# Performance work log

Measured on AMD Instinct MI355X. Metric: run time of the kernel, lower is better.

## Reference

```python
import jax, jax.numpy as jnp
import numpy as np
import math

FACTOR = 5  # module default

def setup_inputs() -> dict:
    key = jax.random.key(0)
    kq, kk, kv, ki = jax.random.split(key, 4)
    B, L, S, H, D = 2, 4096, 4096, 8, 64
    u_part = min(FACTOR * math.ceil(math.log(L)), S)  # 45: sampled keys per query
    return {
        "queries": jax.random.normal(kq, (B, L, H, D), jnp.float32),
        "keys": jax.random.normal(kk, (B, S, H, D), jnp.float32),
        "values": jax.random.normal(kv, (B, S, H, D), jnp.float32),
        "index_sample": jax.random.randint(ki, (L, u_part), 0, S),
    }

def reference(queries, keys, values, index_sample):
    # queries: [B,L,H,D], keys/values: [B,S,H,D], index_sample: [L,u_part]
    B, L, H, D = queries.shape
    S = keys.shape[1]
    Q = jnp.transpose(queries, (0, 2, 1, 3))  # [B,H,L,D]
    K = jnp.transpose(keys, (0, 2, 1, 3))     # [B,H,S,D]
    V = jnp.transpose(values, (0, 2, 1, 3))   # [B,H,S,D]
    U_part = min(FACTOR * math.ceil(math.log(S)), L)  # n_top queries (static)

    # --- _prob_QK: sample keys, sparsity measure M, top-k queries ---
    K_sample = K[:, :, index_sample, :]  # gather -> [B,H,L,u_part,D]
    QK_sample = jnp.einsum('bhld,bhlud->bhlu', Q, K_sample)  # [B,H,L,u_part]
    M = QK_sample.max(axis=-1) - QK_sample.sum(axis=-1) / S  # [B,H,L]
    _, M_top = jax.lax.top_k(M, U_part)                      # [B,H,U_part]
    Q_reduce = jnp.take_along_axis(Q, M_top[..., None], axis=2)  # [B,H,U_part,D]
    scores = jnp.einsum('bhud,bhsd->bhus', Q_reduce, K)          # [B,H,U_part,S]

    # --- mask_flag=False branch: plain scaled softmax attention ---
    scale = 1.0 / math.sqrt(D)
    attn = jax.nn.softmax(scores * scale, axis=-1)  # [B,H,U_part,S]
    context = jnp.einsum('bhus,bhsd->bhud', attn, V)  # [B,H,U_part,D]
    return context, attn
```

## Files before the change

kernel.cpp:

```cpp
#include <hip/hip_runtime.h>

#define BB 2
#define LL 4096
#define SS 4096
#define HH 8
#define DD 64
#define UU 45
#define SCALE 0.125f

__global__ __launch_bounds__(256) void k_compute_M(
    const float* __restrict__ q, const float* __restrict__ k,
    const int* __restrict__ idx, float* __restrict__ M) {
  __shared__ int sidx[16 * UU];
  int tid = threadIdx.x;
  int bh = blockIdx.x & 15;
  int l0 = (blockIdx.x >> 4) << 4;
  for (int i = tid; i < 16 * UU; i += 256) sidx[i] = idx[(long)l0 * UU + i];
  __syncthreads();

  int slot = tid >> 4;
  int sub  = tid & 15;
  int l = l0 + slot;
  int b = bh >> 3, h = bh & 7;

  const float4* qp = (const float4*)(q + (((long)b * LL + l) * HH + h) * DD);
  float4 qq = qp[sub];
  const float* kb = k + (long)b * SS * HH * DD + h * DD;

  float mx = -INFINITY, sm = 0.f;
  #pragma unroll 5
  for (int u = 0; u < UU; ++u) {
    int s = sidx[slot * UU + u];
    float4 kk4 = ((const float4*)(kb + (long)s * (HH * DD)))[sub];
    float p = qq.x * kk4.x + qq.y * kk4.y + qq.z * kk4.z + qq.w * kk4.w;
    #pragma unroll
    for (int off = 8; off; off >>= 1) p += __shfl_xor(p, off, 16);
    mx = fmaxf(mx, p);
    sm += p;
  }
  if (sub == 0) M[(long)bh * LL + l] = mx - sm * (1.0f / SS);
}

__global__ __launch_bounds__(256) void k_topk(
    const float* __restrict__ M, int* __restrict__ Mtop) {
  __shared__ unsigned keys[LL];
  __shared__ int hist[256];
  __shared__ int wsum[4];
  __shared__ int sh_bin, sh_gtwin;
  __shared__ int ccount, ecount;
  __shared__ unsigned cand_key[64];
  __shared__ int cand_idx[64];
  __shared__ int elist[LL];

  int bh = blockIdx.x, tid = threadIdx.x;
  int lane = tid & 63, w = tid >> 6;
  const float* m = M + (long)bh * LL;
  for (int i = tid; i < LL; i += 256) {
    union { float f; unsigned u; } cv; cv.f = m[i];
    keys[i] = (cv.u & 0x80000000u) ? ~cv.u : (cv.u | 0x80000000u);
  }
  if (tid == 0) { ccount = 0; ecount = 0; }
  __syncthreads();

  unsigned prefix = 0, pmask = 0;
  int need = UU, above = 0;

  for (int shift = 24; shift >= 0; shift -= 8) {
    hist[tid] = 0;
    __syncthreads();
    #pragma unroll
    for (int j = 0; j < 16; ++j) {
      unsigned kk = keys[tid + (j << 8)];
      if ((kk & pmask) == prefix) atomicAdd(&hist[(kk >> shift) & 255], 1);
    }
    __syncthreads();
    int v = hist[tid];
    int sfx = v;
    #pragma unroll
    for (int st = 1; st < 64; st <<= 1) {
      int o = __shfl_down(sfx, st, 64);
      if (lane + st < 64) sfx += o;
    }
    if (lane == 0) wsum[w] = sfx;
    __syncthreads();
    for (int t = w + 1; t < 4; ++t) sfx += wsum[t];
    int gt = sfx - v;
    if (gt < need && sfx >= need) {
      sh_bin = tid;
      sh_gtwin = gt;
    }
    __syncthreads();
    prefix |= ((unsigned)sh_bin << shift);
    pmask  |= (255u << shift);
    need  -= sh_gtwin;
    above += sh_gtwin;
    __syncthreads();
  }
  unsigned T = prefix;

  #pragma unroll
  for (int j = 0; j < 16; ++j) {
    int i = tid + (j << 8);
    unsigned kk = keys[i];
    if (kk > T)      { int p = atomicAdd(&ccount, 1); cand_key[p] = kk; cand_idx[p] = i; }
    else if (kk == T){ int p = atomicAdd(&ecount, 1); elist[p] = i; }
  }
  __syncthreads();
  int nc = ccount, ne = ecount;
  for (int t = tid; t < nc; t += 256) {
    unsigned kk = cand_key[t]; int ii = cand_idx[t]; int r = 0;
    for (int j = 0; j < nc; ++j)
      r += (cand_key[j] > kk) || (cand_key[j] == kk && cand_idx[j] < ii);
    Mtop[bh * UU + r] = ii;
  }
  for (int t = tid; t < ne; t += 256) {
    int ii = elist[t]; int r = 0;
    for (int j = 0; j < ne; ++j) r += (elist[j] < ii);
    if (r < need) Mtop[bh * UU + above + r] = ii;
  }
}

__global__ __launch_bounds__(256) void k_scores(
    const float* __restrict__ q, const float* __restrict__ k,
    const int* __restrict__ Mtop, float* __restrict__ attn) {
  __shared__ float qr[UU * DD];
  int bh = blockIdx.y;
  int b = bh >> 3, h = bh & 7;
  for (int i = threadIdx.x; i < UU * DD; i += 256) {
    int u = i >> 6, d = i & 63;
    int l = Mtop[bh * UU + u];
    qr[i] = q[(((long)b * LL + l) * HH + h) * DD + d];
  }
  __syncthreads();
  int s = blockIdx.x * 256 + threadIdx.x;
  float4 kr[16];
  const float4* kp = (const float4*)(k + (((long)b * SS + s) * HH + h) * DD);
  #pragma unroll
  for (int j = 0; j < 16; ++j) kr[j] = kp[j];
  for (int u = 0; u < UU; ++u) {
    const float4* qp = (const float4*)(qr + u * DD);
    float acc = 0.f;
    #pragma unroll
    for (int j = 0; j < 16; ++j) {
      float4 qq = qp[j];
      acc += qq.x * kr[j].x + qq.y * kr[j].y + qq.z * kr[j].z + qq.w * kr[j].w;
    }
    attn[((long)bh * UU + u) * SS + s] = acc * SCALE;
  }
}

__global__ __launch_bounds__(256) void k_softmax(float* __restrict__ attn) {
  __shared__ float red[256];
  long row = blockIdx.x;
  float* a = attn + row * SS;
  float v[16];
  float mx = -INFINITY;
  #pragma unroll
  for (int j = 0; j < 16; ++j) {
    v[j] = a[j * 256 + threadIdx.x];
    mx = fmaxf(mx, v[j]);
  }
  red[threadIdx.x] = mx;
  __syncthreads();
  for (int st = 128; st; st >>= 1) {
    if (threadIdx.x < st) red[threadIdx.x] = fmaxf(red[threadIdx.x], red[threadIdx.x + st]);
    __syncthreads();
  }
  mx = red[0];
  __syncthreads();
  float sm = 0.f;
  #pragma unroll
  for (int j = 0; j < 16; ++j) {
    v[j] = __expf(v[j] - mx);
    sm += v[j];
  }
  red[threadIdx.x] = sm;
  __syncthreads();
  for (int st = 128; st; st >>= 1) {
    if (threadIdx.x < st) red[threadIdx.x] += red[threadIdx.x + st];
    __syncthreads();
  }
  float inv = 1.0f / red[0];
  #pragma unroll
  for (int j = 0; j < 16; ++j) a[j * 256 + threadIdx.x] = v[j] * inv;
}

__global__ __launch_bounds__(256) void k_context_part(
    const float* __restrict__ attn, const float* __restrict__ v,
    float* __restrict__ part, int nch) {
  __shared__ float smem[4 * UU * DD];
  int ch = blockIdx.x, bh = blockIdx.y;
  int b = bh >> 3, h = bh & 7;
  int tid = threadIdx.x;
  int ln = tid & 63, w = tid >> 6;
  int chunk = SS / nch;
  int s0 = ch * chunk;
  int nsub = chunk >> 7;

  float acc[UU];
  #pragma unroll
  for (int u = 0; u < UU; ++u) acc[u] = 0.f;

  const float* vb = v + (long)b * SS * HH * DD + h * DD + ln;

  for (int sub = 0; sub < nsub; ++sub) {
    int sb = s0 + (sub << 7);
    __syncthreads();
    for (int i = tid; i < UU * 128; i += 256) {
      int u = i >> 7, si = i & 127;
      smem[si * 52 + u] = attn[((long)bh * UU + u) * SS + sb + si];
    }
    __syncthreads();
    #pragma unroll 2
    for (int j = 0; j < 32; ++j) {
      int sl = (j << 2) + w;
      float vd = vb[(long)(sb + sl) * (HH * DD)];
      const float* ar = smem + sl * 52;
      #pragma unroll
      for (int g = 0; g < 11; ++g) {
        float4 aa = *(const float4*)(ar + g * 4);
        acc[g * 4 + 0] += aa.x * vd;
        acc[g * 4 + 1] += aa.y * vd;
        acc[g * 4 + 2] += aa.z * vd;
        acc[g * 4 + 3] += aa.w * vd;
      }
      acc[44] += ar[44] * vd;
    }
  }

  __syncthreads();
  #pragma unroll
  for (int u = 0; u < UU; ++u) smem[(w * UU + u) * DD + ln] = acc[u];
  __syncthreads();
  long base = ((long)bh * nch + ch) * (UU * DD);
  for (int i = tid; i < UU * DD; i += 256)
    part[base + i] = smem[i] + smem[UU * DD + i] + smem[2 * UU * DD + i] + smem[3 * UU * DD + i];
}

__global__ __launch_bounds__(256) void k_context_reduce(
    const float* __restrict__ part, float* __restrict__ ctx, int nch) {
  int g = blockIdx.x * 256 + threadIdx.x;
  int bh = g / (UU * DD);
  int r  = g - bh * (UU * DD);
  float s = 0.f;
  for (int ch = 0; ch < nch; ++ch)
    s += part[((long)bh * nch + ch) * (UU * DD) + r];
  ctx[g] = s;
}

__global__ __launch_bounds__(256) void k_context_fb(
    const float* __restrict__ attn, const float* __restrict__ v,
    float* __restrict__ ctx) {
  __shared__ float red[4][DD];
  int row = blockIdx.x;
  int bh = row / UU;
  int b = bh >> 3, h = bh & 7;
  int lane = threadIdx.x & 63;
  int grp = threadIdx.x >> 6;
  const float* a = attn + (long)row * SS;
  float acc = 0.f;
  for (int s = grp; s < SS; s += 4)
    acc += a[s] * v[(((long)b * SS + s) * HH + h) * DD + lane];
  red[grp][lane] = acc;
  __syncthreads();
  if (grp == 0)
    ctx[(long)row * DD + lane] = red[0][lane] + red[1][lane] + red[2][lane] + red[3][lane];
}

extern "C" void kernel_launch(void* const* d_in, const int* in_sizes, int n_in,
                              void* d_out, int out_size, void* d_ws, size_t ws_size,
                              hipStream_t stream) {
  const float* q   = (const float*)d_in[0];
  const float* k   = (const float*)d_in[1];
  const float* v   = (const float*)d_in[2];
  const int*   idx = (const int*)d_in[3];

  float* out  = (float*)d_out;
  float* ctx  = out;
  float* attn = out + (long)BB * HH * UU * DD;

  float* M    = attn;
  int*   Mtop = (int*)ctx;

  k_compute_M<<<BB * HH * LL / 16, 256, 0, stream>>>(q, k, idx, M);
  k_topk<<<BB * HH, 256, 0, stream>>>(M, Mtop);
  k_scores<<<dim3(SS / 256, BB * HH), 256, 0, stream>>>(q, k, Mtop, attn);
  k_softmax<<<BB * HH * UU, 256, 0, stream>>>(attn);

  size_t per_chunk = (size_t)BB * HH * UU * DD * sizeof(float);
  int nch = 0;
  for (int c = 32; c >= 1; c >>= 1)
    if (ws_size >= per_chunk * (size_t)c) { nch = c; break; }
  if (nch) {
    k_context_part<<<dim3(nch, BB * HH), 256, 0, stream>>>(attn, v, (float*)d_ws, nch);
    k_context_reduce<<<(BB * HH * UU * DD) / 256, 256, 0, stream>>>((const float*)d_ws, ctx, nch);
  } else {
    k_context_fb<<<BB * HH * UU, 256, 0, stream>>>(attn, v, ctx);
  }
}
```

Measured before the change: 122.7 us.

## Fuse softmax into score and context kernels via per-tile max/sum stats

Replaces the separate softmax pass with per-tile online-softmax statistics (max and exp-sum) computed in the score kernel. The context kernel merges the stats, normalizes attention on the fly while staging it into shared memory, and writes the normalized probabilities back. This removes one kernel launch and a full read-modify-write pass over the attention matrix. In exchange the score kernel gets extra shared memory for a score tile, and the workspace layout now reserves a fixed offset for the stats.

Measured after the change: 128.7 us. 1.05x slower.

```diff
diff --git a/kernel.cpp b/kernel.cpp
--- a/kernel.cpp
+++ b/kernel.cpp
@@ -7,6 +7,7 @@
 #define DD 64
 #define UU 45
 #define SCALE 0.125f
+#define NTILE 16
 
 __global__ __launch_bounds__(256) void k_compute_M(
     const float* __restrict__ q, const float* __restrict__ k,
@@ -120,6 +121,53 @@
   }
 }
 
+__global__ __launch_bounds__(256) void k_scores_stats(
+    const float* __restrict__ q, const float* __restrict__ k,
+    const int* __restrict__ Mtop, float* __restrict__ attn,
+    float2* __restrict__ stats) {
+  __shared__ float qr[UU * DD];
+  __shared__ float sc[UU][260];
+  int bh = blockIdx.y, tile = blockIdx.x;
+  int b = bh >> 3, h = bh & 7;
+  int tid = threadIdx.x;
+  for (int i = tid; i < UU * DD; i += 256) {
+    int u = i >> 6, d = i & 63;
+    int l = Mtop[bh * UU + u];
+    qr[i] = q[(((long)b * LL + l) * HH + h) * DD + d];
+  }
+  __syncthreads();
+  int s = tile * 256 + tid;
+  float4 kr[16];
+  const float4* kp = (const float4*)(k + (((long)b * SS + s) * HH + h) * DD);
+  #pragma unroll
+  for (int j = 0; j < 16; ++j) kr[j] = kp[j];
+  for (int u = 0; u < UU; ++u) {
+    const float4* qp = (const float4*)(qr + u * DD);
+    float acc = 0.f;
+    #pragma unroll
+    for (int j = 0; j < 16; ++j) {
+      float4 qq = qp[j];
+      acc += qq.x * kr[j].x + qq.y * kr[j].y + qq.z * kr[j].z + qq.w * kr[j].w;
+    }
+    acc *= SCALE;
+    sc[u][tid] = acc;
+    attn[((long)bh * UU + u) * SS + s] = acc;
+  }
+  __syncthreads();
+  int lane = tid & 63, w = tid >> 6;
+  for (int u = w; u < UU; u += 4) {
+    float a0 = sc[u][lane],       a1 = sc[u][lane + 64];
+    float a2 = sc[u][lane + 128], a3 = sc[u][lane + 192];
+    float mx = fmaxf(fmaxf(a0, a1), fmaxf(a2, a3));
+    #pragma unroll
+    for (int off = 32; off; off >>= 1) mx = fmaxf(mx, __shfl_xor(mx, off, 64));
+    float e = __expf(a0 - mx) + __expf(a1 - mx) + __expf(a2 - mx) + __expf(a3 - mx);
+    #pragma unroll
+    for (int off = 32; off; off >>= 1) e += __shfl_xor(e, off, 64);
+    if (lane == 0) stats[((long)bh * UU + u) * NTILE + tile] = make_float2(mx, e);
+  }
+}
+
 __global__ __launch_bounds__(256) void k_scores(
     const float* __restrict__ q, const float* __restrict__ k,
     const int* __restrict__ Mtop, float* __restrict__ attn) {
@@ -186,9 +234,10 @@
 }
 
 __global__ __launch_bounds__(256) void k_context_part(
-    const float* __restrict__ attn, const float* __restrict__ v,
-    float* __restrict__ part, int nch) {
+    float* __restrict__ attn, const float2* __restrict__ stats,
+    const float* __restrict__ v, float* __restrict__ part, int nch) {
   __shared__ float smem[4 * UU * DD];
+  __shared__ float gm[UU], gi[UU];
   int ch = blockIdx.x, bh = blockIdx.y;
   int b = bh >> 3, h = bh & 7;
   int tid = threadIdx.x;
@@ -197,6 +246,17 @@
   int s0 = ch * chunk;
   int nsub = chunk >> 7;
 
+  if (tid < UU) {
+    const float2* st = stats + ((long)bh * UU + tid) * NTILE;
+    float mx = -INFINITY;
+    #pragma unroll
+    for (int t = 0; t < NTILE; ++t) mx = fmaxf(mx, st[t].x);
+    float sm = 0.f;
+    #pragma unroll
+    for (int t = 0; t < NTILE; ++t) sm += st[t].y * __expf(st[t].x - mx);
+    gm[tid] = mx; gi[tid] = 1.0f / sm;
+  }
+
   float acc[UU];
   #pragma unroll
   for (int u = 0; u < UU; ++u) acc[u] = 0.f;
@@ -208,7 +268,10 @@
     __syncthreads();
     for (int i = tid; i < UU * 128; i += 256) {
       int u = i >> 7, si = i & 127;
-      smem[si * 52 + u] = attn[((long)bh * UU + u) * SS + sb + si];
+      long ga = ((long)bh * UU + u) * SS + sb + si;
+      float p = __expf(attn[ga] - gm[u]) * gi[u];
+      smem[si * 52 + u] = p;
+      attn[ga] = p;
     }
     __syncthreads();
     #pragma unroll 2
@@ -284,17 +347,24 @@
 
   k_compute_M<<<BB * HH * LL / 16, 256, 0, stream>>>(q, k, idx, M);
   k_topk<<<BB * HH, 256, 0, stream>>>(M, Mtop);
-  k_scores<<<dim3(SS / 256, BB * HH), 256, 0, stream>>>(q, k, Mtop, attn);
-  k_softmax<<<BB * HH * UU, 256, 0, stream>>>(attn);
-
-  size_t per_chunk = (size_t)BB * HH * UU * DD * sizeof(float);
+
+  size_t stats_bytes = (size_t)BB * HH * UU * NTILE * sizeof(float2);
+  size_t stats_off   = 131072;
+  size_t per_chunk   = (size_t)BB * HH * UU * DD * sizeof(float);
   int nch = 0;
   for (int c = 32; c >= 1; c >>= 1)
-    if (ws_size >= per_chunk * (size_t)c) { nch = c; break; }
+    if (ws_size >= stats_off + per_chunk * (size_t)c) { nch = c; break; }
+
   if (nch) {
-    k_context_part<<<dim3(nch, BB * HH), 256, 0, stream>>>(attn, v, (float*)d_ws, nch);
-    k_context_reduce<<<(BB * HH * UU * DD) / 256, 256, 0, stream>>>((const float*)d_ws, ctx, nch);
+    float2* stats = (float2*)d_ws;
+    float*  part  = (float*)((char*)d_ws + stats_off);
+    k_scores_stats<<<dim3(NTILE, BB * HH), 256, 0, stream>>>(q, k, Mtop, attn, stats);
+    k_context_part<<<dim3(nch, BB * HH), 256, 0, stream>>>(attn, stats, v, part, nch);
+    k_context_reduce<<<(BB * HH * UU * DD) / 256, 256, 0, stream>>>(part, ctx, nch);
   } else {
+    k_scores<<<dim3(SS / 256, BB * HH), 256, 0, stream>>>(q, k, Mtop, attn);
+    k_softmax<<<BB * HH * UU, 256, 0, stream>>>(attn);
     k_context_fb<<<BB * HH * UU, 256, 0, stream>>>(attn, v, ctx);
   }
-}
+  (void)stats_bytes;
+}
```

## Fuse scores, chunked softmax and context into one flash-style kernel with epilogue

Applied to the files above, without the earlier changes.

Replaces the separate scores, softmax, context-partial and reduce kernels with one fused kernel. Each block computes a 128-key chunk of scores, a local max and sum, unnormalized probabilities and partial context. A combined epilogue kernel then rescales attn rows and merges the partial contexts using the per-chunk stats. This removes the round trips of the attn matrix through global memory and two kernel launches. In exchange the attn rows are rewritten in a second pass, and the fused kernel launches only 512 blocks with heavy register use.

Measured after the change: 108.6 us, median of 2. 11.5% less time.

```diff
diff --git a/kernel.cpp b/kernel.cpp
--- a/kernel.cpp
+++ b/kernel.cpp
@@ -7,6 +7,8 @@
 #define DD 64
 #define UU 45
 #define SCALE 0.125f
+#define NCH 32
+#define CHK 128
 
 __global__ __launch_bounds__(256) void k_compute_M(
     const float* __restrict__ q, const float* __restrict__ k,
@@ -120,6 +122,157 @@
   }
 }
 
+__global__ __launch_bounds__(256) void k_fused(
+    const float* __restrict__ q, const float* __restrict__ k,
+    const float* __restrict__ v, const int* __restrict__ Mtop,
+    float* __restrict__ attn, float* __restrict__ part,
+    float2* __restrict__ stats) {
+  __shared__ float smem[4 * UU * DD];
+  __shared__ float gm[UU], gl[UU];
+  float* qr = smem;
+  float* sp = smem + UU * DD;
+
+  int ch = blockIdx.x, bh = blockIdx.y;
+  int b = bh >> 3, h = bh & 7;
+  int tid = threadIdx.x;
+  int lane = tid & 63, w = tid >> 6;
+  int s0 = ch * CHK;
+
+  for (int i = tid; i < UU * DD; i += 256) {
+    int u = i >> 6, d = i & 63;
+    int l = Mtop[bh * UU + u];
+    qr[i] = q[(((long)b * LL + l) * HH + h) * DD + d];
+  }
+  __syncthreads();
+
+  {
+    int sl = tid & 127, uh = tid >> 7;
+    float4 kr[16];
+    const float4* kp = (const float4*)(k + (((long)b * SS + s0 + sl) * HH + h) * DD);
+    #pragma unroll
+    for (int j = 0; j < 16; ++j) kr[j] = kp[j];
+    int u0 = uh ? 23 : 0, u1 = uh ? UU : 23;
+    for (int u = u0; u < u1; ++u) {
+      const float4* qp = (const float4*)(qr + u * DD);
+      float acc = 0.f;
+      #pragma unroll
+      for (int j = 0; j < 16; ++j) {
+        float4 qq = qp[j];
+        acc += qq.x * kr[j].x + qq.y * kr[j].y + qq.z * kr[j].z + qq.w * kr[j].w;
+      }
+      sp[sl * 52 + u] = acc * SCALE;
+    }
+  }
+  __syncthreads();
+
+  for (int u = w; u < UU; u += 4) {
+    float a0 = sp[lane * 52 + u];
+    float a1 = sp[(lane + 64) * 52 + u];
+    float mx = fmaxf(a0, a1);
+    #pragma unroll
+    for (int off = 32; off; off >>= 1) mx = fmaxf(mx, __shfl_xor(mx, off, 64));
+    if (lane == 0) gm[u] = mx;
+  }
+  __syncthreads();
+  for (int i = tid; i < UU * CHK; i += 256) {
+    int u = i >> 7, sl = i & 127;
+    float p = __expf(sp[sl * 52 + u] - gm[u]);
+    sp[sl * 52 + u] = p;
+    attn[((long)bh * UU + u) * SS + s0 + sl] = p;
+  }
+  __syncthreads();
+  for (int u = w; u < UU; u += 4) {
+    float a0 = sp[lane * 52 + u];
+    float a1 = sp[(lane + 64) * 52 + u];
+    float e = a0 + a1;
+    #pragma unroll
+    for (int off = 32; off; off >>= 1) e += __shfl_xor(e, off, 64);
+    if (lane == 0) gl[u] = e;
+  }
+
+  float acc[UU];
+  #pragma unroll
+  for (int u = 0; u < UU; ++u) acc[u] = 0.f;
+  const float* vb = v + (long)b * SS * HH * DD + h * DD + lane;
+  #pragma unroll 2
+  for (int j = 0; j < 32; ++j) {
+    int sl = (j << 2) + w;
+    float vd = vb[(long)(s0 + sl) * (HH * DD)];
+    const float* ar = sp + sl * 52;
+    #pragma unroll
+    for (int g = 0; g < 11; ++g) {
+      float4 aa = *(const float4*)(ar + g * 4);
+      acc[g * 4 + 0] += aa.x * vd;
+      acc[g * 4 + 1] += aa.y * vd;
+      acc[g * 4 + 2] += aa.z * vd;
+      acc[g * 4 + 3] += aa.w * vd;
+    }
+    acc[44] += ar[44] * vd;
+  }
+
+  __syncthreads();
+  #pragma unroll
+  for (int u = 0; u < UU; ++u) smem[(w * UU + u) * DD + lane] = acc[u];
+  __syncthreads();
+  long base = ((long)bh * NCH + ch) * (UU * DD);
+  for (int i = tid; i < UU * DD; i += 256)
+    part[base + i] = smem[i] + smem[UU * DD + i] + smem[2 * UU * DD + i] + smem[3 * UU * DD + i];
+  if (tid < UU)
+    stats[((long)bh * UU + tid) * NCH + ch] = make_float2(gm[tid], gl[tid]);
+}
+
+__global__ __launch_bounds__(256) void k_epilogue(
+    const float2* __restrict__ stats, const float* __restrict__ part,
+    float* __restrict__ attn, float* __restrict__ ctx) {
+  __shared__ float f[NCH];
+  __shared__ float2 st_s[NCH];
+  int bid = blockIdx.x, tid = threadIdx.x;
+  if (bid < BB * HH * UU) {
+    long row = bid;
+    const float2* st = stats + row * NCH;
+    if (tid < NCH) st_s[tid] = st[tid];
+    __syncthreads();
+    if (tid == 0) {
+      float M = -INFINITY;
+      #pragma unroll
+      for (int c = 0; c < NCH; ++c) M = fmaxf(M, st_s[c].x);
+      float L = 0.f;
+      #pragma unroll
+      for (int c = 0; c < NCH; ++c) L += st_s[c].y * __expf(st_s[c].x - M);
+      float inv = 1.0f / L;
+      #pragma unroll
+      for (int c = 0; c < NCH; ++c) f[c] = __expf(st_s[c].x - M) * inv;
+    }
+    __syncthreads();
+    float4* a = (float4*)(attn + row * SS);
+    #pragma unroll
+    for (int g = 0; g < 4; ++g) {
+      int i4 = g * 256 + tid;
+      float ff = f[i4 >> 5];
+      float4 vv = a[i4];
+      vv.x *= ff; vv.y *= ff; vv.z *= ff; vv.w *= ff;
+      a[i4] = vv;
+    }
+  } else {
+    int e = (bid - BB * HH * UU) * 256 + tid;
+    int bh = e / (UU * DD);
+    int r = e - bh * (UU * DD);
+    int u = r >> 6;
+    const float2* st = stats + ((long)bh * UU + u) * NCH;
+    float M = -INFINITY;
+    #pragma unroll
+    for (int c = 0; c < NCH; ++c) M = fmaxf(M, st[c].x);
+    float L = 0.f, s = 0.f;
+    #pragma unroll
+    for (int c = 0; c < NCH; ++c) {
+      float ee = __expf(st[c].x - M);
+      L += st[c].y * ee;
+      s += part[((long)bh * NCH + c) * (UU * DD) + r] * ee;
+    }
+    ctx[e] = s / L;
+  }
+}
+
 __global__ __launch_bounds__(256) void k_scores(
     const float* __restrict__ q, const float* __restrict__ k,
     const int* __restrict__ Mtop, float* __restrict__ attn) {
@@ -183,69 +336,6 @@
   float inv = 1.0f / red[0];
   #pragma unroll
   for (int j = 0; j < 16; ++j) a[j * 256 + threadIdx.x] = v[j] * inv;
-}
-
-__global__ __launch_bounds__(256) void k_context_part(
-    const float* __restrict__ attn, const float* __restrict__ v,
-    float* __restrict__ part, int nch) {
-  __shared__ float smem[4 * UU * DD];
-  int ch = blockIdx.x, bh = blockIdx.y;
-  int b = bh >> 3, h = bh & 7;
-  int tid = threadIdx.x;
-  int ln = tid & 63, w = tid >> 6;
-  int chunk = SS / nch;
-  int s0 = ch * chunk;
-  int nsub = chunk >> 7;
-
-  float acc[UU];
-  #pragma unroll
-  for (int u = 0; u < UU; ++u) acc[u] = 0.f;
-
-  const float* vb = v + (long)b * SS * HH * DD + h * DD + ln;
-
-  for (int sub = 0; sub < nsub; ++sub) {
-    int sb = s0 + (sub << 7);
-    __syncthreads();
-    for (int i = tid; i < UU * 128; i += 256) {
-      int u = i >> 7, si = i & 127;
-      smem[si * 52 + u] = attn[((long)bh * UU + u) * SS + sb + si];
-    }
-    __syncthreads();
-    #pragma unroll 2
-    for (int j = 0; j < 32; ++j) {
-      int sl = (j << 2) + w;
-      float vd = vb[(long)(sb + sl) * (HH * DD)];
-      const float* ar = smem + sl * 52;
-      #pragma unroll
-      for (int g = 0; g < 11; ++g) {
-        float4 aa = *(const float4*)(ar + g * 4);
-        acc[g * 4 + 0] += aa.x * vd;
-        acc[g * 4 + 1] += aa.y * vd;
-        acc[g * 4 + 2] += aa.z * vd;
-        acc[g * 4 + 3] += aa.w * vd;
-      }
-      acc[44] += ar[44] * vd;
-    }
-  }
-
-  __syncthreads();
-  #pragma unroll
-  for (int u = 0; u < UU; ++u) smem[(w * UU + u) * DD + ln] = acc[u];
-  __syncthreads();
-  long base = ((long)bh * nch + ch) * (UU * DD);
-  for (int i = tid; i < UU * DD; i += 256)
-    part[base + i] = smem[i] + smem[UU * DD + i] + smem[2 * UU * DD + i] + smem[3 * UU * DD + i];
-}
-
-__global__ __launch_bounds__(256) void k_context_reduce(
-    const float* __restrict__ part, float* __restrict__ ctx, int nch) {
-  int g = blockIdx.x * 256 + threadIdx.x;
-  int bh = g / (UU * DD);
-  int r  = g - bh * (UU * DD);
-  float s = 0.f;
-  for (int ch = 0; ch < nch; ++ch)
-    s += part[((long)bh * nch + ch) * (UU * DD) + r];
-  ctx[g] = s;
 }
 
 __global__ __launch_bounds__(256) void k_context_fb(
@@ -284,17 +374,18 @@
 
   k_compute_M<<<BB * HH * LL / 16, 256, 0, stream>>>(q, k, idx, M);
   k_topk<<<BB * HH, 256, 0, stream>>>(M, Mtop);
-  k_scores<<<dim3(SS / 256, BB * HH), 256, 0, stream>>>(q, k, Mtop, attn);
-  k_softmax<<<BB * HH * UU, 256, 0, stream>>>(attn);
-
-  size_t per_chunk = (size_t)BB * HH * UU * DD * sizeof(float);
-  int nch = 0;
-  for (int c = 32; c >= 1; c >>= 1)
-    if (ws_size >= per_chunk * (size_t)c) { nch = c; break; }
-  if (nch) {
-    k_context_part<<<dim3(nch, BB * HH), 256, 0, stream>>>(attn, v, (float*)d_ws, nch);
-    k_context_reduce<<<(BB * HH * UU * DD) / 256, 256, 0, stream>>>((const float*)d_ws, ctx, nch);
+
+  size_t part_bytes  = (size_t)BB * HH * NCH * UU * DD * sizeof(float);
+  size_t stats_bytes = (size_t)BB * HH * UU * NCH * sizeof(float2);
+  if (ws_size >= part_bytes + stats_bytes) {
+    float*  part  = (float*)d_ws;
+    float2* stats = (float2*)((char*)d_ws + part_bytes);
+    k_fused<<<dim3(NCH, BB * HH), 256, 0, stream>>>(q, k, v, Mtop, attn, part, stats);
+    int nctx = (BB * HH * UU * DD) / 256;
+    k_epilogue<<<BB * HH * UU + nctx, 256, 0, stream>>>(stats, part, attn, ctx);
   } else {
+    k_scores<<<dim3(SS / 256, BB * HH), 256, 0, stream>>>(q, k, Mtop, attn);
+    k_softmax<<<BB * HH * UU, 256, 0, stream>>>(attn);
     k_context_fb<<<BB * HH * UU, 256, 0, stream>>>(attn, v, ctx);
   }
 }
```
